# Kernel optimization log

Hardware: AMD Instinct MI355X
Metric: run time of the kernel (lower is better)

## Reference

```python
import jax, jax.numpy as jnp
import numpy as np

NQ, NKV, HD, SW = 32, 8, 64, 512  # n_q_heads, n_kv_heads, head_dim, sliding_window (layer index 0 -> window active)
QM = NQ // NKV


def _rope_tables(L):
    # inv_freq: (1/1024)^linspace over head_dim//4 freqs, padded with head_dim//4 zeros -> head_dim//2
    inv_freq = (1.0 / 1024.0) ** jnp.linspace(0.0, 1.0, HD // 4)
    inv_freq = jnp.concatenate([inv_freq, jnp.zeros(HD // 4)])
    theta = jnp.arange(L, dtype=jnp.float32)[:, None] * inv_freq[None, :]  # (L, HD//2)
    return jnp.cos(theta), jnp.sin(theta)


def _apply_rope(x, cos, sin):
    x1, x2 = jnp.split(x, 2, axis=-1)
    return jnp.concatenate([x1 * cos + x2 * sin, -x1 * sin + x2 * cos], axis=-1)


def setup_inputs() -> dict:
    key = jax.random.key(0)
    k1, k2, k3 = jax.random.split(key, 3)
    B, L, D = 1, 2048, 2048
    x = jax.random.normal(k1, (B, L, D), jnp.float32)
    W_qkv = jax.random.normal(k2, (D, (NQ + 2 * NKV) * HD), jnp.float32) * 0.02
    W_out = jax.random.normal(k3, (NQ * HD, D), jnp.float32) * 0.02
    s = jnp.zeros((1, NKV, QM), jnp.float32)  # attention-sink logits (zero-init param)
    return {"x": x, "W_qkv": W_qkv, "W_out": W_out, "s": s}


def reference(x, W_qkv, W_out, s):
    B, L, D = x.shape
    proj = x @ W_qkv
    q, k, v = jnp.split(proj, (NQ * HD, (NQ + NKV) * HD), axis=-1)
    cos, sin = _rope_tables(L)
    q = _apply_rope(q.reshape(B, L, NKV, QM, HD), cos[None, :, None, None, :], sin[None, :, None, None, :])
    k = _apply_rope(k.reshape(B, L, NKV, HD), cos[None, :, None, :], sin[None, :, None, :])
    v = v.reshape(B, L, NKV, HD)
    sm_scale = 1.0 / jnp.sqrt(jnp.float32(HD))
    # scores: (B, NKV, QM, L, L) -- GQA: K shared across QM query heads (avoids explicit broadcast_to)
    attn = jnp.einsum('bqhmd,bkhd->bhmqk', q, k) * sm_scale
    q_pos = jnp.arange(L)[:, None]
    k_pos = jnp.arange(L)[None, :]
    mask = (q_pos >= k_pos) & (q_pos < k_pos + SW)  # causal AND within sliding window
    # Faithful to source: where(mask, -inf, attn) (mask polarity exactly as in the original module)
    attn = jnp.where(mask, -jnp.inf, attn)
    sink = jnp.broadcast_to(s[:, :, :, None, None], attn.shape[:-1] + (1,))
    w = jax.nn.softmax(jnp.concatenate([attn, sink], axis=-1), axis=-1)[..., :-1]
    out = jnp.einsum('bhmqk,bkhd->bqhmd', w, v).reshape(B, L, NQ * HD)
    return out @ W_out
```

## Files before the change

### kernel.cpp

```cpp
#include <hip/hip_runtime.h>
#include <hip/hip_bf16.h>
#include <math.h>

#define L_SEQ 2048
#define DMODEL 2048
#define PROJW 3072
#define NQH 32
#define NKVH 8
#define HD 64
#define SW 512

typedef __attribute__((ext_vector_type(8))) short bf16x8;
typedef __attribute__((ext_vector_type(4))) float f32x4;

__device__ __forceinline__ ushort f2bf(float x) {
    __hip_bfloat16 h = __float2bfloat16(x);
    return *reinterpret_cast<ushort*>(&h);
}
__device__ __forceinline__ float bf2f(ushort u) {
    __hip_bfloat16 h = *reinterpret_cast<__hip_bfloat16*>(&u);
    return __bfloat162float(h);
}

__device__ __forceinline__ void glds16(const void* g, void* l) {
    __builtin_amdgcn_global_load_lds(
        (__attribute__((address_space(1))) void*)(void*)g,
        (__attribute__((address_space(3))) void*)l, 16, 0, 0);
}

__global__ void rope_tables_kernel(float* __restrict__ cosT, float* __restrict__ sinT) {
    int pos = blockIdx.x * blockDim.x + threadIdx.x;
    if (pos >= L_SEQ) return;
    #pragma unroll
    for (int j = 0; j < 32; ++j) {
        float c, s;
        if (j < 16) {
            float t = (float)j * (1.0f / 15.0f);
            float freq = powf(1.0f / 1024.0f, t);
            float th = (float)pos * freq;
            sincosf(th, &s, &c);
        } else {
            c = 1.0f; s = 0.0f;
        }
        cosT[pos * 32 + j] = c;
        sinT[pos * 32 + j] = s;
    }
}

__global__ __launch_bounds__(256) void split_rm_kernel(const float* __restrict__ A,
                                                       ushort* __restrict__ hi,
                                                       ushort* __restrict__ lo) {
    int i = (blockIdx.x * 256 + threadIdx.x) * 4;
    float4 v = *reinterpret_cast<const float4*>(&A[i]);
    float vv[4] = {v.x, v.y, v.z, v.w};
    ushort h[4], l[4];
    #pragma unroll
    for (int j = 0; j < 4; ++j) {
        h[j] = f2bf(vv[j]);
        l[j] = f2bf(vv[j] - bf2f(h[j]));
    }
    *reinterpret_cast<ushort4*>(&hi[i]) = make_ushort4(h[0], h[1], h[2], h[3]);
    *reinterpret_cast<ushort4*>(&lo[i]) = make_ushort4(l[0], l[1], l[2], l[3]);
}

__global__ __launch_bounds__(256) void split_t_kernel(const float* __restrict__ W,
                                                      ushort* __restrict__ hi,
                                                      ushort* __restrict__ lo,
                                                      int K, int N) {
    __shared__ float t[32][33];
    int n0 = blockIdx.x * 32, k0 = blockIdx.y * 32;
    int tx = threadIdx.x & 31, ty = threadIdx.x >> 5;
    #pragma unroll
    for (int r = 0; r < 32; r += 8)
        t[ty + r][tx] = W[(size_t)(k0 + ty + r) * N + n0 + tx];
    __syncthreads();
    #pragma unroll
    for (int r = 0; r < 32; r += 8) {
        float v = t[tx][ty + r];
        ushort h = f2bf(v);
        ushort l = f2bf(v - bf2f(h));
        size_t o = (size_t)(n0 + ty + r) * K + k0 + tx;
        hi[o] = h;
        lo[o] = l;
    }
}

#define GBK 32

__global__ __launch_bounds__(256) void gemm_bf16x2_kernel(
    const ushort* __restrict__ Ahi, const ushort* __restrict__ Alo,
    const ushort* __restrict__ Bhi, const ushort* __restrict__ Blo,
    float* __restrict__ C, int M, int N, int K)
{
    __shared__ __align__(16) ushort sAh[128 * 32];
    __shared__ __align__(16) ushort sAl[128 * 32];
    __shared__ __align__(16) ushort sBh[128 * 32];
    __shared__ __align__(16) ushort sBl[128 * 32];

    const int tid = threadIdx.x;
    const int w = tid >> 6, lane = tid & 63;
    const int bm = blockIdx.y * 128, bn = blockIdx.x * 128;
    const int wr = w >> 1, wc = w & 1;

    f32x4 acc[4][4];
    #pragma unroll
    for (int i = 0; i < 4; ++i)
        #pragma unroll
        for (int j = 0; j < 4; ++j)
            acc[i][j] = (f32x4){0.0f, 0.0f, 0.0f, 0.0f};

    const int q0 = w * 128 + lane;
    const int q1 = q0 + 64;
    const int r0 = q0 >> 2, r1 = q1 >> 2;
    const int ks0 = ((q0 & 3) ^ (r0 & 3)) * 8;
    const int ks1 = ((q1 & 3) ^ (r1 & 3)) * 8;
    const ushort* gAh0 = Ahi + (size_t)(bm + r0) * K + ks0;
    const ushort* gAh1 = Ahi + (size_t)(bm + r1) * K + ks1;
    const ushort* gAl0 = Alo + (size_t)(bm + r0) * K + ks0;
    const ushort* gAl1 = Alo + (size_t)(bm + r1) * K + ks1;
    const ushort* gBh0 = Bhi + (size_t)(bn + r0) * K + ks0;
    const ushort* gBh1 = Bhi + (size_t)(bn + r1) * K + ks1;
    const ushort* gBl0 = Blo + (size_t)(bn + r0) * K + ks0;
    const ushort* gBl1 = Blo + (size_t)(bn + r1) * K + ks1;
    ushort* dAh0 = sAh + (w * 2 + 0) * 512;
    ushort* dAh1 = sAh + (w * 2 + 1) * 512;
    ushort* dAl0 = sAl + (w * 2 + 0) * 512;
    ushort* dAl1 = sAl + (w * 2 + 1) * 512;
    ushort* dBh0 = sBh + (w * 2 + 0) * 512;
    ushort* dBh1 = sBh + (w * 2 + 1) * 512;
    ushort* dBl0 = sBl + (w * 2 + 0) * 512;
    ushort* dBl1 = sBl + (w * 2 + 1) * 512;

    const int kg = lane >> 4;
    const int fr = lane & 15;

    for (int k0 = 0; k0 < K; k0 += GBK) {
        __syncthreads();
        glds16(gAh0 + k0, dAh0);
        glds16(gAh1 + k0, dAh1);
        glds16(gBh0 + k0, dBh0);
        glds16(gBh1 + k0, dBh1);
        glds16(gAl0 + k0, dAl0);
        glds16(gAl1 + k0, dAl1);
        glds16(gBl0 + k0, dBl0);
        glds16(gBl1 + k0, dBl1);
        __syncthreads();

        bf16x8 ah[4], al[4], bh[4], bl[4];
        #pragma unroll
        for (int i = 0; i < 4; ++i) {
            int row = wr * 64 + i * 16 + fr;
            int off = row * 32 + ((kg ^ (row & 3)) * 8);
            ah[i] = *reinterpret_cast<const bf16x8*>(&sAh[off]);
            al[i] = *reinterpret_cast<const bf16x8*>(&sAl[off]);
        }
        #pragma unroll
        for (int j = 0; j < 4; ++j) {
            int row = wc * 64 + j * 16 + fr;
            int off = row * 32 + ((kg ^ (row & 3)) * 8);
            bh[j] = *reinterpret_cast<const bf16x8*>(&sBh[off]);
            bl[j] = *reinterpret_cast<const bf16x8*>(&sBl[off]);
        }
        #pragma unroll
        for (int i = 0; i < 4; ++i)
            #pragma unroll
            for (int j = 0; j < 4; ++j) {
                acc[i][j] = __builtin_amdgcn_mfma_f32_16x16x32_bf16(ah[i], bh[j], acc[i][j], 0, 0, 0);
                acc[i][j] = __builtin_amdgcn_mfma_f32_16x16x32_bf16(ah[i], bl[j], acc[i][j], 0, 0, 0);
                acc[i][j] = __builtin_amdgcn_mfma_f32_16x16x32_bf16(al[i], bh[j], acc[i][j], 0, 0, 0);
            }
    }

    const int rq = (lane >> 4) * 4;
    #pragma unroll
    for (int i = 0; i < 4; ++i)
        #pragma unroll
        for (int j = 0; j < 4; ++j) {
            #pragma unroll
            for (int q = 0; q < 4; ++q) {
                C[(size_t)(bm + wr * 64 + i * 16 + rq + q) * N + bn + wc * 64 + j * 16 + fr]
                    = acc[i][j][q];
            }
        }
}

__global__ __launch_bounds__(256) void prep_qk_kernel(
    const float* __restrict__ proj,
    const float* __restrict__ cosT, const float* __restrict__ sinT,
    ushort* __restrict__ Qh, ushort* __restrict__ Ql,
    ushort* __restrict__ Kh, ushort* __restrict__ Kl)
{
    int pos = blockIdx.x;
    const float* row = proj + (size_t)pos * PROJW;
    const float* ct = cosT + pos * 32;
    const float* st = sinT + pos * 32;
    int t = threadIdx.x;
    #pragma unroll
    for (int it = 0; it < 4; ++it) {
        int p = t + it * 256;
        int head = p >> 5, d = p & 31;
        float x1 = row[head * HD + d], x2 = row[head * HD + d + 32];
        float c = ct[d], s = st[d];
        float y1 = x1 * c + x2 * s;
        float y2 = -x1 * s + x2 * c;
        size_t o = ((size_t)head * L_SEQ + pos) * HD + d;
        ushort h1 = f2bf(y1); Qh[o] = h1;      Ql[o] = f2bf(y1 - bf2f(h1));
        ushort h2 = f2bf(y2); Qh[o + 32] = h2; Ql[o + 32] = f2bf(y2 - bf2f(h2));
    }
    {
        int head = t >> 5, d = t & 31;
        float x1 = row[DMODEL + head * HD + d], x2 = row[DMODEL + head * HD + d + 32];
        float c = ct[d], s = st[d];
        float y1 = x1 * c + x2 * s;
        float y2 = -x1 * s + x2 * c;
        size_t o = ((size_t)head * L_SEQ + pos) * HD + d;
        ushort h1 = f2bf(y1); Kh[o] = h1;      Kl[o] = f2bf(y1 - bf2f(h1));
        ushort h2 = f2bf(y2); Kh[o + 32] = h2; Kl[o + 32] = f2bf(y2 - bf2f(h2));
    }
}

__global__ __launch_bounds__(256) void prep_v_kernel(const float* __restrict__ proj,
                                                     ushort* __restrict__ Vth,
                                                     ushort* __restrict__ Vtl)
{
    __shared__ float tile[64][65];
    int h = blockIdx.y, p0 = blockIdx.x * 64;
    int t = threadIdx.x;
    {
        int r = t >> 2, c0 = (t & 3) * 16;
        const float* src = proj + (size_t)(p0 + r) * PROJW + DMODEL + NKVH * HD + h * HD + c0;
        #pragma unroll
        for (int i = 0; i < 16; i += 4) {
            float4 v = *reinterpret_cast<const float4*>(src + i);
            tile[r][c0 + i + 0] = v.x;
            tile[r][c0 + i + 1] = v.y;
            tile[r][c0 + i + 2] = v.z;
            tile[r][c0 + i + 3] = v.w;
        }
    }
    __syncthreads();
    {
        int d = t >> 2, c0 = (t & 3) * 16;
        ushort hh[16], ll[16];
        #pragma unroll
        for (int i = 0; i < 16; ++i) {
            float v = tile[c0 + i][d];
            hh[i] = f2bf(v);
            ll[i] = f2bf(v - bf2f(hh[i]));
        }
        size_t o = ((size_t)h * HD + d) * L_SEQ + p0 + c0;
        #pragma unroll
        for (int i = 0; i < 16; i += 4) {
            *reinterpret_cast<ushort4*>(&Vth[o + i]) = make_ushort4(hh[i], hh[i+1], hh[i+2], hh[i+3]);
            *reinterpret_cast<ushort4*>(&Vtl[o + i]) = make_ushort4(ll[i], ll[i+1], ll[i+2], ll[i+3]);
        }
    }
}

__global__ __launch_bounds__(256, 2) void attn_mfma_kernel(
    const ushort* __restrict__ Qh, const ushort* __restrict__ Ql,
    const ushort* __restrict__ Kh, const ushort* __restrict__ Kl,
    const ushort* __restrict__ Vth, const ushort* __restrict__ Vtl,
    const float* __restrict__ sink,
    ushort* __restrict__ out_hi, ushort* __restrict__ out_lo)
{
    __shared__ ushort Pth[4][32][72];
    __shared__ ushort Ptl[4][32][72];

    const int tid = threadIdx.x;
    const int w = tid >> 6, lane = tid & 63;
    const int fr = lane & 15, g = lane >> 4;
    const int q0 = blockIdx.x * 32;
    const int h = blockIdx.y;
    const int hq = h * 4 + w;

    const ushort* Qb_h = Qh + ((size_t)hq * L_SEQ + q0) * HD;
    const ushort* Qb_l = Ql + ((size_t)hq * L_SEQ + q0) * HD;
    const ushort* Kb_h = Kh + (size_t)h * L_SEQ * HD;
    const ushort* Kb_l = Kl + (size_t)h * L_SEQ * HD;
    const ushort* Vb_h = Vth + (size_t)h * HD * L_SEQ;
    const ushort* Vb_l = Vtl + (size_t)h * HD * L_SEQ;

    bf16x8 qbh[2][2], qbl[2][2];
    #pragma unroll
    for (int j = 0; j < 2; ++j)
        #pragma unroll
        for (int kc = 0; kc < 2; ++kc) {
            size_t o = (size_t)(j * 16 + fr) * HD + kc * 32 + g * 8;
            qbh[j][kc] = *reinterpret_cast<const bf16x8*>(Qb_h + o);
            qbl[j][kc] = *reinterpret_cast<const bf16x8*>(Qb_l + o);
        }

    const float sval = sink[hq];
    float m[2] = {sval, sval};
    float l[2] = {1.0f, 1.0f};
    f32x4 ot[4][2];
    #pragma unroll
    for (int i = 0; i < 4; ++i)
        #pragma unroll
        for (int j = 0; j < 2; ++j)
            ot[i][j] = (f32x4){0.0f, 0.0f, 0.0f, 0.0f};

    for (int k0 = 0; k0 < L_SEQ; k0 += 64) {
        if ((q0 >= k0 + 63) && (q0 + 31 < k0 + SW)) continue;

        bf16x8 kah[4][2], kal[4][2];
        #pragma unroll
        for (int i = 0; i < 4; ++i)
            #pragma unroll
            for (int kc = 0; kc < 2; ++kc) {
                size_t o = (size_t)(k0 + i * 16 + fr) * HD + kc * 32 + g * 8;
                kah[i][kc] = *reinterpret_cast<const bf16x8*>(Kb_h + o);
                kal[i][kc] = *reinterpret_cast<const bf16x8*>(Kb_l + o);
            }

        f32x4 st4[4][2];
        #pragma unroll
        for (int i = 0; i < 4; ++i)
            #pragma unroll
            for (int j = 0; j < 2; ++j)
                st4[i][j] = (f32x4){0.0f, 0.0f, 0.0f, 0.0f};
        #pragma unroll
        for (int i = 0; i < 4; ++i)
            #pragma unroll
            for (int j = 0; j < 2; ++j)
                #pragma unroll
                for (int kc = 0; kc < 2; ++kc) {
                    st4[i][j] = __builtin_amdgcn_mfma_f32_16x16x32_bf16(kah[i][kc], qbh[j][kc], st4[i][j], 0, 0, 0);
                    st4[i][j] = __builtin_amdgcn_mfma_f32_16x16x32_bf16(kah[i][kc], qbl[j][kc], st4[i][j], 0, 0, 0);
                    st4[i][j] = __builtin_amdgcn_mfma_f32_16x16x32_bf16(kal[i][kc], qbh[j][kc], st4[i][j], 0, 0, 0);
                }

        bf16x8 vah[4][2], val[4][2];
        #pragma unroll
        for (int i = 0; i < 4; ++i)
            #pragma unroll
            for (int kc = 0; kc < 2; ++kc) {
                size_t o = (size_t)(i * 16 + fr) * L_SEQ + k0 + kc * 32 + g * 8;
                vah[i][kc] = *reinterpret_cast<const bf16x8*>(Vb_h + o);
                val[i][kc] = *reinterpret_cast<const bf16x8*>(Vb_l + o);
            }

        #pragma unroll
        for (int j = 0; j < 2; ++j) {
            int q = q0 + j * 16 + fr;
            float tm = -INFINITY;
            #pragma unroll
            for (int i = 0; i < 4; ++i)
                #pragma unroll
                for (int r = 0; r < 4; ++r) {
                    int k = k0 + i * 16 + g * 4 + r;
                    float s = st4[i][j][r] * 0.125f;
                    if ((q >= k) && (q < k + SW)) s = -INFINITY;
                    st4[i][j][r] = s;
                    tm = fmaxf(tm, s);
                }
            tm = fmaxf(tm, __shfl_xor(tm, 16));
            tm = fmaxf(tm, __shfl_xor(tm, 32));
            float nm = fmaxf(m[j], tm);
            float al = __expf(m[j] - nm);
            float ps = 0.0f;
            #pragma unroll
            for (int i = 0; i < 4; ++i)
                #pragma unroll
                for (int r = 0; r < 4; ++r) {
                    float p = __expf(st4[i][j][r] - nm);
                    st4[i][j][r] = p;
                    ps += p;
                }
            ps += __shfl_xor(ps, 16);
            ps += __shfl_xor(ps, 32);
            l[j] = l[j] * al + ps;
            m[j] = nm;
            #pragma unroll
            for (int i = 0; i < 4; ++i) ot[i][j] *= al;

            #pragma unroll
            for (int i = 0; i < 4; ++i) {
                ushort ph[4], pl[4];
                #pragma unroll
                for (int r = 0; r < 4; ++r) {
                    float p = st4[i][j][r];
                    ph[r] = f2bf(p);
                    pl[r] = f2bf(p - bf2f(ph[r]));
                }
                *reinterpret_cast<ushort4*>(&Pth[w][j * 16 + fr][i * 16 + g * 4])
                    = make_ushort4(ph[0], ph[1], ph[2], ph[3]);
                *reinterpret_cast<ushort4*>(&Ptl[w][j * 16 + fr][i * 16 + g * 4])
                    = make_ushort4(pl[0], pl[1], pl[2], pl[3]);
            }
        }

        bf16x8 pbh[2][2], pbl[2][2];
        #pragma unroll
        for (int j = 0; j < 2; ++j)
            #pragma unroll
            for (int kc = 0; kc < 2; ++kc) {
                pbh[j][kc] = *reinterpret_cast<const bf16x8*>(&Pth[w][j * 16 + fr][kc * 32 + g * 8]);
                pbl[j][kc] = *reinterpret_cast<const bf16x8*>(&Ptl[w][j * 16 + fr][kc * 32 + g * 8]);
            }

        #pragma unroll
        for (int i = 0; i < 4; ++i)
            #pragma unroll
            for (int j = 0; j < 2; ++j)
                #pragma unroll
                for (int kc = 0; kc < 2; ++kc) {
                    ot[i][j] = __builtin_amdgcn_mfma_f32_16x16x32_bf16(vah[i][kc], pbh[j][kc], ot[i][j], 0, 0, 0);
                    ot[i][j] = __builtin_amdgcn_mfma_f32_16x16x32_bf16(vah[i][kc], pbl[j][kc], ot[i][j], 0, 0, 0);
                    ot[i][j] = __builtin_amdgcn_mfma_f32_16x16x32_bf16(val[i][kc], pbh[j][kc], ot[i][j], 0, 0, 0);
                }
    }

    #pragma unroll
    for (int j = 0; j < 2; ++j) {
        float inv = 1.0f / l[j];
        int q = q0 + j * 16 + fr;
        #pragma unroll
        for (int i = 0; i < 4; ++i) {
            ushort hh[4], ll[4];
            #pragma unroll
            for (int r = 0; r < 4; ++r) {
                float v = ot[i][j][r] * inv;
                hh[r] = f2bf(v);
                ll[r] = f2bf(v - bf2f(hh[r]));
            }
            size_t o = (size_t)q * DMODEL + hq * HD + i * 16 + g * 4;
            *reinterpret_cast<ushort4*>(&out_hi[o]) = make_ushort4(hh[0], hh[1], hh[2], hh[3]);
            *reinterpret_cast<ushort4*>(&out_lo[o]) = make_ushort4(ll[0], ll[1], ll[2], ll[3]);
        }
    }
}

extern "C" void kernel_launch(void* const* d_in, const int* in_sizes, int n_in,
                              void* d_out, int out_size, void* d_ws, size_t ws_size,
                              hipStream_t stream) {
    const float* x     = (const float*)d_in[0];
    const float* W_qkv = (const float*)d_in[1];
    const float* W_out = (const float*)d_in[2];
    const float* s     = (const float*)d_in[3];
    float* outp = (float*)d_out;

    char* ws = (char*)d_ws;
    float*  proj = (float*)ws;  ws += (size_t)L_SEQ * PROJW * 4;
    float*  cosT = (float*)ws;  ws += (size_t)L_SEQ * 32 * 4;
    float*  sinT = (float*)ws;  ws += (size_t)L_SEQ * 32 * 4;
    ushort* xh   = (ushort*)ws; ws += (size_t)L_SEQ * DMODEL * 2;
    ushort* xl   = (ushort*)ws; ws += (size_t)L_SEQ * DMODEL * 2;
    ushort* wqh  = (ushort*)ws; ws += (size_t)PROJW * DMODEL * 2;
    ushort* wql  = (ushort*)ws; ws += (size_t)PROJW * DMODEL * 2;
    ushort* woh  = (ushort*)ws; ws += (size_t)DMODEL * DMODEL * 2;
    ushort* wol  = (ushort*)ws; ws += (size_t)DMODEL * DMODEL * 2;
    ushort* kh   = (ushort*)ws; ws += (size_t)NKVH * L_SEQ * HD * 2;
    ushort* kl   = (ushort*)ws; ws += (size_t)NKVH * L_SEQ * HD * 2;
    ushort* vth  = (ushort*)ws; ws += (size_t)NKVH * HD * L_SEQ * 2;
    ushort* vtl  = (ushort*)ws; ws += (size_t)NKVH * HD * L_SEQ * 2;

    ushort* qh  = xh;
    ushort* ql  = xl;
    ushort* ath = wqh;
    ushort* atl = wql;

    rope_tables_kernel<<<(L_SEQ + 255) / 256, 256, 0, stream>>>(cosT, sinT);

    split_rm_kernel<<<(L_SEQ * DMODEL) / 1024, 256, 0, stream>>>(x, xh, xl);
    split_t_kernel<<<dim3(PROJW / 32, DMODEL / 32), 256, 0, stream>>>(W_qkv, wqh, wql, DMODEL, PROJW);
    split_t_kernel<<<dim3(DMODEL / 32, DMODEL / 32), 256, 0, stream>>>(W_out, woh, wol, DMODEL, DMODEL);

    gemm_bf16x2_kernel<<<dim3(PROJW / 128, L_SEQ / 128), 256, 0, stream>>>(
        xh, xl, wqh, wql, proj, L_SEQ, PROJW, DMODEL);

    prep_qk_kernel<<<L_SEQ, 256, 0, stream>>>(proj, cosT, sinT, qh, ql, kh, kl);
    prep_v_kernel<<<dim3(L_SEQ / 64, NKVH), 256, 0, stream>>>(proj, vth, vtl);

    attn_mfma_kernel<<<dim3(L_SEQ / 32, NKVH), 256, 0, stream>>>(
        qh, ql, kh, kl, vth, vtl, s, ath, atl);

    gemm_bf16x2_kernel<<<dim3(DMODEL / 128, L_SEQ / 128), 256, 0, stream>>>(
        ath, atl, woh, wol, outp, L_SEQ, DMODEL, DMODEL);
}
```

Baseline: 533.6 us.

## Stage K tiles in swizzled shared memory with double buffering and skip masked range

The attention kernel now loads K tiles cooperatively into double-buffered, XOR-swizzled LDS via async global-to-LDS copies, so the four waves share one copy instead of each fetching K from global memory. The key loop iterates only over tiles outside the fully masked band, and masking is applied only on boundary tiles. The softmax scale is folded into Q during RoPE prep, the P scratch buffer uses a swizzled layout to reduce bank conflicts, and the grid is flattened so neighbouring blocks cover different KV heads. In exchange it uses more LDS, which may lower occupancy, and adds a block-wide barrier on every iteration.

```diff
diff --git a/kernel.cpp b/kernel.cpp
--- a/kernel.cpp
+++ b/kernel.cpp
@@ -201,8 +201,8 @@
         int head = p >> 5, d = p & 31;
         float x1 = row[head * HD + d], x2 = row[head * HD + d + 32];
         float c = ct[d], s = st[d];
-        float y1 = x1 * c + x2 * s;
-        float y2 = -x1 * s + x2 * c;
+        float y1 = (x1 * c + x2 * s) * 0.125f;
+        float y2 = (-x1 * s + x2 * c) * 0.125f;
         size_t o = ((size_t)head * L_SEQ + pos) * HD + d;
         ushort h1 = f2bf(y1); Qh[o] = h1;      Ql[o] = f2bf(y1 - bf2f(h1));
         ushort h2 = f2bf(y2); Qh[o + 32] = h2; Ql[o + 32] = f2bf(y2 - bf2f(h2));
@@ -264,14 +264,17 @@
     const float* __restrict__ sink,
     ushort* __restrict__ out_hi, ushort* __restrict__ out_lo)
 {
-    __shared__ ushort Pth[4][32][72];
-    __shared__ ushort Ptl[4][32][72];
+    __shared__ __align__(16) ushort KsH[2][4096];
+    __shared__ __align__(16) ushort KsL[2][4096];
+    __shared__ __align__(16) ushort PtH[4][2048];
+    __shared__ __align__(16) ushort PtL[4][2048];
 
     const int tid = threadIdx.x;
     const int w = tid >> 6, lane = tid & 63;
     const int fr = lane & 15, g = lane >> 4;
-    const int q0 = blockIdx.x * 32;
-    const int h = blockIdx.y;
+    const int bid = blockIdx.x;
+    const int h = bid & 7;
+    const int q0 = (bid >> 3) * 32;
     const int hq = h * 4 + w;
 
     const ushort* Qb_h = Qh + ((size_t)hq * L_SEQ + q0) * HD;
@@ -281,6 +284,26 @@
     const ushort* Vb_h = Vth + (size_t)h * HD * L_SEQ;
     const ushort* Vb_l = Vtl + (size_t)h * HD * L_SEQ;
 
+    int sA = q0 - 480, sB = q0 - 63;
+    int kA = (sA + 63) & ~63; if (kA < 0) kA = 0;
+    int kB = sB & ~63;
+    bool has_skip = (sB >= 0) && (kA <= kB);
+    int n1 = has_skip ? (kA >> 6) : (L_SEQ >> 6);
+    int kResume = has_skip ? (kB + 64) : 0;
+    int nt = n1 + (has_skip ? ((L_SEQ - kResume) >> 6) : 0);
+    #define K0_OF(t) ((t) < n1 ? (t) * 64 : kResume + ((t) - n1) * 64)
+
+    #define STAGE_K(buf, k0s) do {                                                  \
+        _Pragma("unroll")                                                           \
+        for (int qi = 0; qi < 2; ++qi) {                                            \
+            int gq = (w * 2 + qi) * 64 + lane;                                      \
+            int srow = gq >> 3, sc = gq & 7;                                        \
+            size_t soff = (size_t)((k0s) + srow) * HD + ((sc ^ (srow & 7)) * 8);    \
+            glds16(Kb_h + soff, &KsH[buf][(w * 2 + qi) * 512]);                     \
+            glds16(Kb_l + soff, &KsL[buf][(w * 2 + qi) * 512]);                     \
+        }                                                                           \
+    } while (0)
+
     bf16x8 qbh[2][2], qbl[2][2];
     #pragma unroll
     for (int j = 0; j < 2; ++j)
@@ -301,17 +324,23 @@
         for (int j = 0; j < 2; ++j)
             ot[i][j] = (f32x4){0.0f, 0.0f, 0.0f, 0.0f};
 
-    for (int k0 = 0; k0 < L_SEQ; k0 += 64) {
-        if ((q0 >= k0 + 63) && (q0 + 31 < k0 + SW)) continue;
+    STAGE_K(0, K0_OF(0));
+    __syncthreads();
+
+    for (int t = 0; t < nt; ++t) {
+        const int cur = t & 1;
+        if (t + 1 < nt) STAGE_K(cur ^ 1, K0_OF(t + 1));
+        const int k0 = K0_OF(t);
 
         bf16x8 kah[4][2], kal[4][2];
         #pragma unroll
         for (int i = 0; i < 4; ++i)
             #pragma unroll
             for (int kc = 0; kc < 2; ++kc) {
-                size_t o = (size_t)(k0 + i * 16 + fr) * HD + kc * 32 + g * 8;
-                kah[i][kc] = *reinterpret_cast<const bf16x8*>(Kb_h + o);
-                kal[i][kc] = *reinterpret_cast<const bf16x8*>(Kb_l + o);
+                int row = i * 16 + fr;
+                int off = row * 64 + (((kc * 4 + g) ^ (row & 7)) * 8);
+                kah[i][kc] = *reinterpret_cast<const bf16x8*>(&KsH[cur][off]);
+                kal[i][kc] = *reinterpret_cast<const bf16x8*>(&KsL[cur][off]);
             }
 
         f32x4 st4[4][2];
@@ -341,20 +370,30 @@
                 val[i][kc] = *reinterpret_cast<const bf16x8*>(Vb_l + o);
             }
 
+        const bool need_mask = (q0 + 31 >= k0) && (q0 < k0 + 63 + SW);
+
         #pragma unroll
         for (int j = 0; j < 2; ++j) {
             int q = q0 + j * 16 + fr;
             float tm = -INFINITY;
-            #pragma unroll
-            for (int i = 0; i < 4; ++i)
+            if (need_mask) {
                 #pragma unroll
-                for (int r = 0; r < 4; ++r) {
-                    int k = k0 + i * 16 + g * 4 + r;
-                    float s = st4[i][j][r] * 0.125f;
-                    if ((q >= k) && (q < k + SW)) s = -INFINITY;
-                    st4[i][j][r] = s;
-                    tm = fmaxf(tm, s);
-                }
+                for (int i = 0; i < 4; ++i)
+                    #pragma unroll
+                    for (int r = 0; r < 4; ++r) {
+                        int k = k0 + i * 16 + g * 4 + r;
+                        float s = st4[i][j][r];
+                        if ((q >= k) && (q < k + SW)) s = -INFINITY;
+                        st4[i][j][r] = s;
+                        tm = fmaxf(tm, s);
+                    }
+            } else {
+                #pragma unroll
+                for (int i = 0; i < 4; ++i)
+                    #pragma unroll
+                    for (int r = 0; r < 4; ++r)
+                        tm = fmaxf(tm, st4[i][j][r]);
+            }
             tm = fmaxf(tm, __shfl_xor(tm, 16));
             tm = fmaxf(tm, __shfl_xor(tm, 32));
             float nm = fmaxf(m[j], tm);
@@ -375,6 +414,7 @@
             #pragma unroll
             for (int i = 0; i < 4; ++i) ot[i][j] *= al;
 
+            int prow = j * 16 + fr;
             #pragma unroll
             for (int i = 0; i < 4; ++i) {
                 ushort ph[4], pl[4];
@@ -384,10 +424,10 @@
                     ph[r] = f2bf(p);
                     pl[r] = f2bf(p - bf2f(ph[r]));
                 }
-                *reinterpret_cast<ushort4*>(&Pth[w][j * 16 + fr][i * 16 + g * 4])
-                    = make_ushort4(ph[0], ph[1], ph[2], ph[3]);
-                *reinterpret_cast<ushort4*>(&Ptl[w][j * 16 + fr][i * 16 + g * 4])
-                    = make_ushort4(pl[0], pl[1], pl[2], pl[3]);
+                int pc = (i * 2 + (g >> 1)) ^ (prow & 7);
+                int poff = prow * 64 + pc * 8 + (g & 1) * 4;
+                *reinterpret_cast<ushort4*>(&PtH[w][poff]) = make_ushort4(ph[0], ph[1], ph[2], ph[3]);
+                *reinterpret_cast<ushort4*>(&PtL[w][poff]) = make_ushort4(pl[0], pl[1], pl[2], pl[3]);
             }
         }
 
@@ -396,8 +436,10 @@
         for (int j = 0; j < 2; ++j)
             #pragma unroll
             for (int kc = 0; kc < 2; ++kc) {
-                pbh[j][kc] = *reinterpret_cast<const bf16x8*>(&Pth[w][j * 16 + fr][kc * 32 + g * 8]);
-                pbl[j][kc] = *reinterpret_cast<const bf16x8*>(&Ptl[w][j * 16 + fr][kc * 32 + g * 8]);
+                int prow = j * 16 + fr;
+                int off = prow * 64 + (((kc * 4 + g) ^ (prow & 7)) * 8);
+                pbh[j][kc] = *reinterpret_cast<const bf16x8*>(&PtH[w][off]);
+                pbl[j][kc] = *reinterpret_cast<const bf16x8*>(&PtL[w][off]);
             }
 
         #pragma unroll
@@ -410,6 +452,8 @@
                     ot[i][j] = __builtin_amdgcn_mfma_f32_16x16x32_bf16(vah[i][kc], pbl[j][kc], ot[i][j], 0, 0, 0);
                     ot[i][j] = __builtin_amdgcn_mfma_f32_16x16x32_bf16(val[i][kc], pbh[j][kc], ot[i][j], 0, 0, 0);
                 }
+
+        __syncthreads();
     }
 
     #pragma unroll
@@ -430,6 +474,8 @@
             *reinterpret_cast<ushort4*>(&out_lo[o]) = make_ushort4(ll[0], ll[1], ll[2], ll[3]);
         }
     }
+    #undef STAGE_K
+    #undef K0_OF
 }
 
 extern "C" void kernel_launch(void* const* d_in, const int* in_sizes, int n_in,
@@ -473,7 +519,7 @@
     prep_qk_kernel<<<L_SEQ, 256, 0, stream>>>(proj, cosT, sinT, qh, ql, kh, kl);
     prep_v_kernel<<<dim3(L_SEQ / 64, NKVH), 256, 0, stream>>>(proj, vth, vtl);
 
-    attn_mfma_kernel<<<dim3(L_SEQ / 32, NKVH), 256, 0, stream>>>(
+    attn_mfma_kernel<<<(L_SEQ / 32) * NKVH, 256, 0, stream>>>(
         qh, ql, kh, kl, vth, vtl, s, ath, atl);
 
     gemm_bf16x2_kernel<<<dim3(DMODEL / 128, L_SEQ / 128), 256, 0, stream>>>(
```

After: 440.6 us. 1.21x faster.
